# Kernel tuning notes

Measured on AMD Instinct MI355X. Metric: run time of the kernel, lower is better.

The kernel has to match this reference:

```python
import jax, jax.numpy as jnp
import numpy as np

# Constants from the module's __init__ (LIFNodes / RUMNodes / Connection args)
DT = 1.0
TAU = 10.0            # LIF membrane time constant
TC_TRACE = 20.0       # spike-trace time constant (bindsnet default)
REST, RESET, THRESH = -70.0, -65.0, -55.0
ALPHA, BETA = 0.95, 0.8     # RUM hidden leak / threshold-adaptation decay
H_THRESH = 1.0              # hidden firing threshold
NU1_PRE, NU1_POST = 0.001, 0.01    # PostPre STDP rates (input->hidden)
NU2 = 0.0001                        # MSTDP learning rate (hidden->output)
WMIN, WMAX = 0.0, 1.0
REWARD = 1.0
A_PLUS, A_MINUS = 1.0, -1.0         # MSTDP trace amplitudes (bindsnet defaults)
TC_PM = 20.0                        # MSTDP p_plus/p_minus time constant
INPUT_GAIN = 20.0   # scales U[0,1) rates into the LIF operating range (rest->thresh gap = 15 mV)

IN_D, HID_D, OUT_D = 544, 1024, 2048


def setup_inputs() -> dict:
    key = jax.random.key(0)
    k1, k2, k3 = jax.random.split(key, 3)
    x = jax.random.uniform(k1, (IN_D,), dtype=jnp.float32)            # rate-coded input
    w1 = jax.random.uniform(k2, (IN_D, HID_D), dtype=jnp.float32)     # in [wmin, wmax]
    w2 = jax.random.uniform(k3, (HID_D, OUT_D), dtype=jnp.float32)
    return {"x": x, "w1": w1, "w2": w2, "num_timesteps": 500}


def _simulate(x, w1, w2, T):
    decay_v = jnp.float32(np.exp(-DT / TAU))
    decay_tr = jnp.float32(np.exp(-DT / TC_TRACE))
    decay_pm = jnp.float32(np.exp(-DT / TC_PM))
    rates = x * INPUT_GAIN  # constant input current each timestep (rate coding)

    carry = (
        jnp.full((IN_D,), REST, jnp.float32),   # v_in
        jnp.zeros((HID_D,), jnp.float32),        # v_hid
        jnp.full((OUT_D,), REST, jnp.float32),   # v_out
        jnp.zeros((IN_D,), jnp.float32),         # tr_in  (pre trace, PostPre)
        jnp.zeros((HID_D,), jnp.float32),        # tr_hid (post trace, PostPre)
        jnp.zeros((HID_D,), jnp.float32),        # b_hid  (RUM threshold adaptation)
        jnp.zeros((HID_D,), jnp.float32),        # p_plus  (MSTDP pre trace)
        jnp.zeros((OUT_D,), jnp.float32),        # p_minus (MSTDP post trace)
        w1, w2,
    )

    def step(c, _):
        v_in, v_hid, v_out, tr_in, tr_hid, b_hid, p_plus, p_minus, w1c, w2c = c
        # --- input LIF: decay toward rest, integrate rates, spike, reset ---
        v_in = decay_v * (v_in - REST) + REST + rates
        s_in = (v_in >= THRESH).astype(jnp.float32)
        v_in = jnp.where(s_in > 0, RESET, v_in)
        tr_in = jnp.where(s_in > 0, 1.0, tr_in * decay_tr)
        # --- hidden RUM: leaky integration (alpha) + adaptive threshold (beta) ---
        i_hid = s_in @ w1c                                  # [HID]
        v_hid = ALPHA * v_hid + i_hid
        s_hid = (v_hid >= H_THRESH + b_hid).astype(jnp.float32)
        v_hid = jnp.where(s_hid > 0, 0.0, v_hid)
        b_hid = BETA * b_hid + s_hid
        tr_hid_new = jnp.where(s_hid > 0, 1.0, tr_hid * decay_tr)
        # --- output LIF ---
        i_out = s_hid @ w2c                                 # [OUT]
        v_out = decay_v * (v_out - REST) + REST + i_out
        s_out = (v_out >= THRESH).astype(jnp.float32)
        v_out = jnp.where(s_out > 0, RESET, v_out)
        # --- PostPre STDP on w1: potentiate on post spike, depress on pre spike ---
        w1c = jnp.clip(
            w1c + NU1_POST * jnp.outer(tr_in, s_hid) - NU1_PRE * jnp.outer(s_in, tr_hid_new),
            WMIN, WMAX)
        # --- MSTDP on w2: reward-modulated eligibility ---
        p_plus = decay_pm * p_plus + A_PLUS * s_hid
        p_minus = decay_pm * p_minus + A_MINUS * s_out
        elig = jnp.outer(p_plus, s_out) + jnp.outer(s_hid, p_minus)  # [HID, OUT]
        w2c = w2c + NU2 * REWARD * DT * elig
        new_c = (v_in, v_hid, v_out, tr_in, tr_hid_new, b_hid, p_plus, p_minus, w1c, w2c)
        return new_c, s_out

    _, spikes = jax.lax.scan(step, carry, None, length=T)
    return spikes  # [T, OUT_D] float32 spike raster (== stacked monitor recording)


def reference(x, w1, w2, num_timesteps):
    return _simulate(x, w1, w2, num_timesteps)
```

## Files before the change

### kernel.cpp

```cpp
#include <hip/hip_runtime.h>
#include <stdint.h>


#define DECAY_V  0.90483741803595952f
#define DECAY_TR 0.95122942450071403f
#define REST_F   (-70.0f)
#define RESET_F  (-65.0f)
#define THRESH_F (-55.0f)
#define ALPHA_F  (0.95f)
#define BETA_F   (0.8f)
#define NU1_PRE_F  (0.001f)
#define NU1_POST_F (0.01f)
#define NU2_F      (0.0001f)
#define GAIN_F     (20.0f)
#define LOG2D    (-0.072134752044448170f)

static constexpr int IN_D  = 544;
static constexpr int HID_D = 1024;
static constexpr int OUT_D = 2048;
static constexpr int TMAX  = 512;

#define DP1  0.95122942450071403f
#define DP2  0.90483741803595957f
#define DP4  0.81873075307798186f
#define DP8  0.67032004603563930f
#define DP16 0.44932896411722159f
#define DP32 0.20189651799465541f

__device__ __forceinline__ float rdlane(float x, int l) {
    return __builtin_bit_cast(float,
        __builtin_amdgcn_readlane(__builtin_bit_cast(int, x), l));
}

template <int CTRL>
__device__ __forceinline__ float dpp_add(float x) {
    int y = __builtin_amdgcn_update_dpp(0, __builtin_bit_cast(int, x),
                                        CTRL, 0xF, 0xF, true);
    return x + __builtin_bit_cast(float, y);
}

__device__ __forceinline__ float wave_sum64(float x) {
    x = dpp_add<0xB1>(x);
    x = dpp_add<0x4E>(x);
    x = dpp_add<0x114>(x);
    x = dpp_add<0x118>(x);
    x = dpp_add<0x142>(x);
    x = dpp_add<0x143>(x);
    return rdlane(x, 63);
}

__global__ __launch_bounds__(256, 2)
void hidden_kernel(const float* __restrict__ x, const float* __restrict__ w1,
                   const int* __restrict__ Tp, float* __restrict__ Sf)
{
    const int T = Tp[0];
    const int tid = threadIdx.x, lane = tid & 63, wv = tid >> 6;
    const int cp = wv >> 1;
    const int h  = wv & 1;
    const int col = blockIdx.x * 2 + cp;
    const float c0 = REST_F * (1.0f - DECAY_V);
    __shared__ float part[2][4];

    float w[5], vi[5], tr[5], cadd[5];
    #pragma unroll
    for (int k = 0; k < 5; ++k) {
        const int o = 64 * k + lane;
        const int i = 272 * h + o;
        const bool ok = (o < 272);
        w[k]    = ok ? w1[(size_t)i * HID_D + col] : 0.f;
        cadd[k] = c0 + (ok ? x[i] * GAIN_F : 0.f);
        vi[k]   = REST_F;
        tr[k]   = 0.f;
    }
    float v_h = 0.f, b_h = 0.f, tr_h = 0.f;
    const bool writer = (h == 0 && lane == 0);

    auto step = [&](int t, int par) {
        float acc = 0.f, s[5];
        #pragma unroll
        for (int k = 0; k < 5; ++k) {
            const float vv = fmaf(DECAY_V, vi[k], cadd[k]);
            const bool sp = (vv >= THRESH_F);
            vi[k] = sp ? RESET_F : vv;
            s[k]  = sp ? 1.f : 0.f;
            tr[k] = fmaxf(tr[k] * DECAY_TR, s[k]);
            acc   = fmaf(s[k], w[k], acc);
        }
        const float p = wave_sum64(acc);
        if (lane == 0) part[par][wv] = p;
        __syncthreads();
        const float tot = p + part[par][wv ^ 1];
        const float vh2 = fmaf(ALPHA_F, v_h, tot);
        const bool hp = (vh2 >= 1.0f + b_h);
        const float sh = hp ? 1.f : 0.f;
        v_h  = hp ? 0.f : vh2;
        b_h  = fmaf(BETA_F, b_h, sh);
        tr_h = hp ? 1.f : tr_h * DECAY_TR;
        const float apot = hp ? NU1_POST_F : 0.f;
        const float adep = NU1_PRE_F * tr_h;
        #pragma unroll
        for (int k = 0; k < 5; ++k) {
            const float a  = fmaf(apot, tr[k], w[k]);
            const float nw = fmaf(-adep, s[k], a);
            w[k] = __builtin_amdgcn_fmed3f(nw, 0.f, 1.f);
        }
        if (writer) Sf[(size_t)t * HID_D + col] = sh;
    };

    int t = 0;
    for (; t + 1 < T; t += 2) {
        step(t, 0);
        step(t + 1, 1);
    }
    if (t < T) step(t, 0);
}

__global__ void pack_kernel(float* __restrict__ Sf, const int* __restrict__ Tp,
                            unsigned long long* __restrict__ Sb)
{
    const int T = Tp[0];
    const int t = blockIdx.x;
    const int lane = threadIdx.x & 63, wv = threadIdx.x >> 6;
    if (t >= T) {
        ((float4*)(Sf + (size_t)t * HID_D))[threadIdx.x] = make_float4(0.f, 0.f, 0.f, 0.f);
        return;
    }
    #pragma unroll
    for (int q = 0; q < 4; ++q) {
        const int word = wv * 4 + q;
        const float s = Sf[(size_t)t * HID_D + word * 64 + lane];
        const unsigned long long m = __ballot(s > 0.5f);
        if (lane == 0) Sb[(size_t)t * 16 + word] = m;
    }
}

__global__ __launch_bounds__(256)
void gramgemm_kernel(const unsigned long long* __restrict__ Sb,
                     const int* __restrict__ Tp, float* __restrict__ G,
                     const float* __restrict__ Sf, const float* __restrict__ w2,
                     float* __restrict__ AT, int klen)
{
    __shared__ __align__(16) char smem[16640];
    const int b = blockIdx.x, tid = threadIdx.x;
    if (b < 1024) {
        const int by = b >> 5, bx = b & 31;
        if (bx > by) return;
        const int T = Tp[0];
        typedef unsigned long long u64;
        u64 (*tR)[17] = (u64(*)[17])(smem);
        u64 (*uR)[17] = (u64(*)[17])(smem + 2176);
        {
            const int r = tid >> 4, w0 = tid & 15;
            const int trow = by * 16 + r, urow = bx * 16 + r;
            tR[r][w0] = (trow < T) ? Sb[(size_t)trow * 16 + w0] : 0ULL;
            uR[r][w0] = (urow < T) ? Sb[(size_t)urow * 16 + w0] : 0ULL;
        }
        __syncthreads();
        const int tx = tid & 15, ty = tid >> 4;
        const int t = by * 16 + ty, u = bx * 16 + tx;
        if (t < T && u < t) {
            int s = 0;
            #pragma unroll
            for (int w0 = 0; w0 < 16; ++w0) s += __popcll(tR[ty][w0] & uR[tx][w0]);
            G[(size_t)t * TMAX + u] = (float)s;
        }
    } else {
        const int g = b - 1024;
        const int z = g >> 7, r = g & 127;
        const int j0 = (r & 15) * 128, t0 = (r >> 4) * 64;
        const int kbase = z * klen;
        float (*Ss)[68]  = (float(*)[68])(smem);
        float (*Ws)[192] = (float(*)[192])(smem + 4352);
        const int sr = tid >> 2, sq = tid & 3;
        const int wq2 = tid & 31, wr2 = tid >> 5;
        const int wcol = (wq2 >> 1) * 12 + (wq2 & 1) * 4;
        const int tj = tid & 15, tt = tid >> 4;
        const int tjc = tj * 12;

        float acc[4][8];
        #pragma unroll
        for (int a = 0; a < 4; ++a)
            #pragma unroll
            for (int bb = 0; bb < 8; ++bb) acc[a][bb] = 0.f;

        for (int k0 = 0; k0 < klen; k0 += 16) {
            const float4 sv = *(const float4*)&Sf[(size_t)(t0 + sr) * HID_D + kbase + k0 + sq * 4];
            const float4 wa = *(const float4*)&w2[(size_t)(kbase + k0 + wr2) * OUT_D + j0 + wq2 * 4];
            const float4 wb = *(const float4*)&w2[(size_t)(kbase + k0 + wr2 + 8) * OUT_D + j0 + wq2 * 4];
            __syncthreads();
            Ss[sq * 4 + 0][sr] = sv.x;
            Ss[sq * 4 + 1][sr] = sv.y;
            Ss[sq * 4 + 2][sr] = sv.z;
            Ss[sq * 4 + 3][sr] = sv.w;
            *(float4*)&Ws[wr2][wcol] = wa;
            *(float4*)&Ws[wr2 + 8][wcol] = wb;
            __syncthreads();
            #pragma unroll
            for (int kk = 0; kk < 16; ++kk) {
                const float4 a4 = *(const float4*)&Ss[kk][tt * 4];
                const float4 b0 = *(const float4*)&Ws[kk][tjc];
                const float4 b1 = *(const float4*)&Ws[kk][tjc + 4];
                const float aa[4] = {a4.x, a4.y, a4.z, a4.w};
                const float bbv[8] = {b0.x, b0.y, b0.z, b0.w, b1.x, b1.y, b1.z, b1.w};
                #pragma unroll
                for (int ti = 0; ti < 4; ++ti)
                    #pragma unroll
                    for (int jj = 0; jj < 8; ++jj)
                        acc[ti][jj] = fmaf(aa[ti], bbv[jj], acc[ti][jj]);
            }
        }
        #pragma unroll
        for (int jj = 0; jj < 8; ++jj)
            *(float4*)&AT[(size_t)z * OUT_D * TMAX +
                          (size_t)(j0 + tj * 8 + jj) * TMAX + t0 + tt * 4] =
                make_float4(acc[0][jj], acc[1][jj], acc[2][jj], acc[3][jj]);
    }
}

__global__ __launch_bounds__(256)
void mt_kernel(const float* __restrict__ G, const int* __restrict__ Tp,
               float* __restrict__ MT)
{
    const int T = Tp[0];
    const int lane = threadIdx.x & 63;
    const int t = blockIdx.x * 4 + (threadIdx.x >> 6);
    if (t >= T) return;
    const float* Gr = G + (size_t)t * TMAX;
    const float dl1  = exp2f((float)(lane + 1) * LOG2D);
    const float d64l = exp2f((float)(64 - lane) * LOG2D);

    float g[8], kk[8];
    #pragma unroll
    for (int c = 0; c < 8; ++c) {
        const int tau = 64 * c + lane;
        g[c] = (tau < t) ? Gr[tau] : 0.f;
    }
    float kc = 0.f;
    #pragma unroll
    for (int c = 7; c >= 0; --c) {
        float k = g[c], u;
        u = __shfl_down(k, 1, 64);  if (lane < 63) k = fmaf(DP1, u, k);
        u = __shfl_down(k, 2, 64);  if (lane < 62) k = fmaf(DP2, u, k);
        u = __shfl_down(k, 4, 64);  if (lane < 60) k = fmaf(DP4, u, k);
        u = __shfl_down(k, 8, 64);  if (lane < 56) k = fmaf(DP8, u, k);
        u = __shfl_down(k, 16, 64); if (lane < 48) k = fmaf(DP16, u, k);
        u = __shfl_down(k, 32, 64); if (lane < 32) k = fmaf(DP32, u, k);
        k = fmaf(d64l, kc, k);
        kk[c] = k;
        kc = rdlane(k, 0);
    }
    float hc = 0.f;
    #pragma unroll
    for (int c = 0; c < 8; ++c) {
        float h = g[c], u;
        u = __shfl_up(h, 1, 64);  if (lane >= 1)  h = fmaf(DP1, u, h);
        u = __shfl_up(h, 2, 64);  if (lane >= 2)  h = fmaf(DP2, u, h);
        u = __shfl_up(h, 4, 64);  if (lane >= 4)  h = fmaf(DP4, u, h);
        u = __shfl_up(h, 8, 64);  if (lane >= 8)  h = fmaf(DP8, u, h);
        u = __shfl_up(h, 16, 64); if (lane >= 16) h = fmaf(DP16, u, h);
        u = __shfl_up(h, 32, 64); if (lane >= 32) h = fmaf(DP32, u, h);
        h = fmaf(dl1, hc, h);
        const int tau = 64 * c + lane;
        if (tau < t) MT[(size_t)tau * TMAX + t] = NU2_F * (h - kk[c]);
        hc = rdlane(h, 63);
    }
}

template <int C>
__device__ __forceinline__ void out_chunk(
    const float* __restrict__ AT, const float* __restrict__ MT,
    float (&hs)[8], float& v, float* __restrict__ out,
    int j, int lane, int w, int T, int nparts, float* __restrict__ LD)
{
    __syncthreads();
    constexpr int t0 = 64 * C;
    const int rem = T - t0;
    const int mtv = (rem < 64) ? rem : 64;
    float av = AT[(size_t)j * TMAX + t0 + lane];
    #pragma unroll
    for (int p = 1; p < 4; ++p)
        if (p < nparts)
            av += AT[(size_t)p * OUT_D * TMAX + (size_t)j * TMAX + t0 + lane];
    const bool hasNext = (C + 1 < 8) && (64 * (C + 1) < T);
    if (hasNext) {
        float* dst = LD + ((C + 1) & 1) * 4096;
        const float* src = MT + (size_t)(64 * (C + 1)) * TMAX + 64 * (C + 1) + lane;
        #pragma unroll
        for (int rr = 0; rr < 16; ++rr) {
            const int r = w * 16 + rr;
            const float vv = src[(size_t)r * TMAX];
            dst[r * 64 + lane] = (r < lane) ? vv : 0.f;
        }
    }
    const float* ldb = LD + (C & 1) * 4096;
    const float cc = REST_F * (1.0f - DECAY_V);
    float acc = hs[C];
    float sreg = 0.f;

    auto sstep = [&](int tt, float& m, int reload) {
        const float iv = rdlane(av + acc, tt);
        const float vd = fmaf(DECAY_V, v, cc) + iv;
        const bool sp = (vd >= THRESH_F);
        const float so = sp ? 1.f : 0.f;
        v = sp ? RESET_F : vd;
        sreg = (lane == tt) ? so : sreg;
        acc = fmaf(so, m, acc);
        if (reload < 64) m = ldb[reload * 64 + lane];
    };

    if (rem >= 64) {
        float m0 = ldb[lane], m1 = ldb[64 + lane],
              m2 = ldb[128 + lane], m3 = ldb[192 + lane];
        #pragma unroll 1
        for (int tt = 0; tt < 64; tt += 4) {
            sstep(tt,     m0, tt + 4);
            sstep(tt + 1, m1, tt + 5);
            sstep(tt + 2, m2, tt + 6);
            sstep(tt + 3, m3, tt + 7);
        }
    } else {
        float m0 = ldb[lane];
        float m1 = (mtv > 1) ? ldb[64 + lane] : 0.f;
        for (int tt = 0; tt < mtv; ++tt) {
            const float mv = m0;
            m0 = m1;
            if (tt + 2 < mtv) m1 = ldb[(tt + 2) * 64 + lane];
            const float iv = rdlane(av + acc, tt);
            const float vd = fmaf(DECAY_V, v, cc) + iv;
            const bool sp = (vd >= THRESH_F);
            const float so = sp ? 1.f : 0.f;
            v = sp ? RESET_F : vd;
            sreg = (lane == tt) ? so : sreg;
            acc = fmaf(so, mv, acc);
        }
    }
    if (lane < mtv) out[(size_t)(t0 + lane) * OUT_D + j] = sreg;

    if (hasNext) {
        #pragma unroll 4
        for (int tt = 0; tt < 64; ++tt) {
            const float s = rdlane(sreg, tt);
            const float* Mrow = MT + (size_t)(t0 + tt) * TMAX + lane;
            #pragma unroll
            for (int K = C + 1; K < 8; ++K)
                hs[K] = fmaf(s, Mrow[64 * K], hs[K]);
        }
    }
}

__global__ __launch_bounds__(256, 2)
void out_kernel(const float* __restrict__ AT, const float* __restrict__ MT,
                const int* __restrict__ Tp, float* __restrict__ out, int nparts)
{
    const int T = Tp[0];
    const int tid = threadIdx.x, lane = tid & 63, w = tid >> 6;
    const int j = blockIdx.x * 4 + w;
    __shared__ float LD[2 * 4096];

    float hs[8];
    #pragma unroll
    for (int k = 0; k < 8; ++k) hs[k] = 0.f;
    float v = REST_F;

    {
        const float* src = MT + lane;
        #pragma unroll
        for (int rr = 0; rr < 16; ++rr) {
            const int r = w * 16 + rr;
            const float vv = src[(size_t)r * TMAX];
            LD[r * 64 + lane] = (r < lane) ? vv : 0.f;
        }
    }
    out_chunk<0>(AT, MT, hs, v, out, j, lane, w, T, nparts, LD);
    if (T >  64) out_chunk<1>(AT, MT, hs, v, out, j, lane, w, T, nparts, LD);
    if (T > 128) out_chunk<2>(AT, MT, hs, v, out, j, lane, w, T, nparts, LD);
    if (T > 192) out_chunk<3>(AT, MT, hs, v, out, j, lane, w, T, nparts, LD);
    if (T > 256) out_chunk<4>(AT, MT, hs, v, out, j, lane, w, T, nparts, LD);
    if (T > 320) out_chunk<5>(AT, MT, hs, v, out, j, lane, w, T, nparts, LD);
    if (T > 384) out_chunk<6>(AT, MT, hs, v, out, j, lane, w, T, nparts, LD);
    if (T > 448) out_chunk<7>(AT, MT, hs, v, out, j, lane, w, T, nparts, LD);
}

extern "C" void kernel_launch(void* const* d_in, const int* in_sizes, int n_in,
                              void* d_out, int out_size, void* d_ws, size_t ws_size,
                              hipStream_t stream) {
    const float* x  = (const float*)d_in[0];
    const float* w1 = (const float*)d_in[1];
    const float* w2 = (const float*)d_in[2];
    const int*   Tp = (const int*)d_in[3];
    float* out = (float*)d_out;
    char* ws = (char*)d_ws;
    unsigned long long* Sb = (unsigned long long*)(ws);
    float* G  = (float*)(ws + 65536);
    float* MT = (float*)(ws + 65536 + 1048576);
    float* Sf = (float*)(ws + 65536 + 2 * 1048576);
    float* AT = (float*)(ws + 65536 + 4 * 1048576);
    const size_t base  = 65536 + 4 * 1048576;
    const int nparts = (ws_size >= base + 4 * 4194304) ? 4
                     : (ws_size >= base + 2 * 4194304) ? 2 : 1;
    const int klen = 1024 / nparts;

    hipLaunchKernelGGL(hidden_kernel, dim3(HID_D / 2), dim3(256), 0, stream, x, w1, Tp, Sf);
    hipLaunchKernelGGL(pack_kernel,   dim3(TMAX), dim3(256), 0, stream, Sf, Tp, Sb);
    hipLaunchKernelGGL(gramgemm_kernel, dim3(1024 + 128 * nparts), dim3(256), 0, stream,
                       Sb, Tp, G, Sf, w2, AT, klen);
    hipLaunchKernelGGL(mt_kernel,     dim3(128), dim3(256), 0, stream, G, Tp, MT);
    hipLaunchKernelGGL(out_kernel,    dim3(OUT_D / 4), dim3(256), 0, stream, AT, MT, Tp, out, nparts);
}
```

Measured before the change: 275.4 us.

## Precompute input-layer spikes in a separate kernel and prefetch them in hidden kernel

```diff
diff --git a/kernel.cpp b/kernel.cpp
--- a/kernel.cpp
+++ b/kernel.cpp
@@ -19,6 +19,7 @@
 static constexpr int HID_D = 1024;
 static constexpr int OUT_D = 2048;
 static constexpr int TMAX  = 512;
+static constexpr int SROW  = 640;
 
 #define DP1  0.95122942450071403f
 #define DP2  0.90483741803595957f
@@ -49,8 +50,30 @@
     return rdlane(x, 63);
 }
 
+__global__ __launch_bounds__(640)
+void input_kernel(const float* __restrict__ x, const int* __restrict__ Tp,
+                  float* __restrict__ Sfin)
+{
+    const int tid = threadIdx.x;
+    const int T = Tp[0];
+    const bool real = (tid < IN_D);
+    const int slot = (tid < 272) ? tid
+                   : real        ? tid + 48
+                   : (tid < 592) ? tid - 272
+                                 : tid;
+    const float cadd = REST_F * (1.0f - DECAY_V) +
+                       (real ? x[tid] * GAIN_F : -1000.0f);
+    float v = REST_F;
+    for (int t = 0; t < T; ++t) {
+        const float vv = fmaf(DECAY_V, v, cadd);
+        const bool sp = (vv >= THRESH_F);
+        v = sp ? RESET_F : vv;
+        Sfin[(size_t)t * SROW + slot] = (real && sp) ? 1.f : 0.f;
+    }
+}
+
 __global__ __launch_bounds__(256, 2)
-void hidden_kernel(const float* __restrict__ x, const float* __restrict__ w1,
+void hidden_kernel(const float* __restrict__ Sfin, const float* __restrict__ w1,
                    const int* __restrict__ Tp, float* __restrict__ Sf)
 {
     const int T = Tp[0];
@@ -58,31 +81,30 @@
     const int cp = wv >> 1;
     const int h  = wv & 1;
     const int col = blockIdx.x * 2 + cp;
-    const float c0 = REST_F * (1.0f - DECAY_V);
     __shared__ float part[2][4];
 
-    float w[5], vi[5], tr[5], cadd[5];
+    float w[5], tr[5];
     #pragma unroll
     for (int k = 0; k < 5; ++k) {
         const int o = 64 * k + lane;
-        const int i = 272 * h + o;
-        const bool ok = (o < 272);
-        w[k]    = ok ? w1[(size_t)i * HID_D + col] : 0.f;
-        cadd[k] = c0 + (ok ? x[i] * GAIN_F : 0.f);
-        vi[k]   = REST_F;
-        tr[k]   = 0.f;
+        w[k]  = (o < 272) ? w1[(size_t)(272 * h + o) * HID_D + col] : 0.f;
+        tr[k] = 0.f;
     }
     float v_h = 0.f, b_h = 0.f, tr_h = 0.f;
     const bool writer = (h == 0 && lane == 0);
-
-    auto step = [&](int t, int par) {
-        float acc = 0.f, s[5];
+    const float* __restrict__ sbase = Sfin + 320 * h + lane;
+
+    float s0[5], s1[5], s2[5], s3[5];
+    auto ld = [&](float (&d)[5], int trow) {
+        const int tc = (trow < TMAX) ? trow : TMAX - 1;
+        const float* p = sbase + (size_t)tc * SROW;
+        #pragma unroll
+        for (int k = 0; k < 5; ++k) d[k] = p[64 * k];
+    };
+    auto step = [&](int t, int par, float (&s)[5]) {
+        float acc = 0.f;
         #pragma unroll
         for (int k = 0; k < 5; ++k) {
-            const float vv = fmaf(DECAY_V, vi[k], cadd[k]);
-            const bool sp = (vv >= THRESH_F);
-            vi[k] = sp ? RESET_F : vv;
-            s[k]  = sp ? 1.f : 0.f;
             tr[k] = fmaxf(tr[k] * DECAY_TR, s[k]);
             acc   = fmaf(s[k], w[k], acc);
         }
@@ -107,12 +129,17 @@
         if (writer) Sf[(size_t)t * HID_D + col] = sh;
     };
 
+    ld(s0, 0); ld(s1, 1); ld(s2, 2); ld(s3, 3);
     int t = 0;
-    for (; t + 1 < T; t += 2) {
-        step(t, 0);
-        step(t + 1, 1);
-    }
-    if (t < T) step(t, 0);
+    for (; t + 3 < T; t += 4) {
+        step(t,     0, s0); ld(s0, t + 4);
+        step(t + 1, 1, s1); ld(s1, t + 5);
+        step(t + 2, 0, s2); ld(s2, t + 6);
+        step(t + 3, 1, s3); ld(s3, t + 7);
+    }
+    if (t < T)     step(t,     0, s0);
+    if (t + 1 < T) step(t + 1, 1, s1);
+    if (t + 2 < T) step(t + 2, 0, s2);
 }
 
 __global__ void pack_kernel(float* __restrict__ Sf, const int* __restrict__ Tp,
@@ -390,17 +417,19 @@
     const int*   Tp = (const int*)d_in[3];
     float* out = (float*)d_out;
     char* ws = (char*)d_ws;
-    unsigned long long* Sb = (unsigned long long*)(ws);
-    float* G  = (float*)(ws + 65536);
-    float* MT = (float*)(ws + 65536 + 1048576);
-    float* Sf = (float*)(ws + 65536 + 2 * 1048576);
-    float* AT = (float*)(ws + 65536 + 4 * 1048576);
-    const size_t base  = 65536 + 4 * 1048576;
+    float* Sfin = (float*)(ws);
+    unsigned long long* Sb = (unsigned long long*)(ws + 1310720);
+    float* G  = (float*)(ws + 1310720 + 65536);
+    float* MT = (float*)(ws + 1310720 + 65536 + 1048576);
+    float* Sf = (float*)(ws + 1310720 + 65536 + 2 * 1048576);
+    float* AT = (float*)(ws + 1310720 + 65536 + 2 * 1048576 + 2097152);
+    const size_t base = 1310720 + 65536 + 2 * 1048576 + 2097152;
     const int nparts = (ws_size >= base + 4 * 4194304) ? 4
                      : (ws_size >= base + 2 * 4194304) ? 2 : 1;
     const int klen = 1024 / nparts;
 
-    hipLaunchKernelGGL(hidden_kernel, dim3(HID_D / 2), dim3(256), 0, stream, x, w1, Tp, Sf);
+    hipLaunchKernelGGL(input_kernel,  dim3(1), dim3(640), 0, stream, x, Tp, Sfin);
+    hipLaunchKernelGGL(hidden_kernel, dim3(HID_D / 2), dim3(256), 0, stream, Sfin, w1, Tp, Sf);
     hipLaunchKernelGGL(pack_kernel,   dim3(TMAX), dim3(256), 0, stream, Sf, Tp, Sb);
     hipLaunchKernelGGL(gramgemm_kernel, dim3(1024 + 128 * nparts), dim3(256), 0, stream,
                        Sb, Tp, G, Sf, w2, AT, klen);
```

Result: slower. 287.3 us (median of 2 runs) (+4.3%).
